# Performance work log

Measured on AMD Instinct MI355X. Metric: run time of the kernel, lower is better.

Reference implementation:

```python
import jax, jax.numpy as jnp
import numpy as np

B, S, D, E, K = 4, 2048, 1024, 8, 2
DF = 4 * D


def setup_inputs() -> dict:
    key = jax.random.key(0)
    ks = jax.random.split(key, 7)
    x = jax.random.normal(ks[0], (B, S, D), dtype=jnp.float32)
    Wr = jax.random.normal(ks[1], (D, E), dtype=jnp.float32) * 0.02
    br = jnp.zeros((E,), dtype=jnp.float32)
    W1 = jax.random.normal(ks[2], (E, D, DF), dtype=jnp.float32) * 0.02
    b1 = jnp.zeros((E, DF), dtype=jnp.float32)
    W2 = jax.random.normal(ks[3], (E, DF, D), dtype=jnp.float32) * 0.02
    b2 = jnp.zeros((E, D), dtype=jnp.float32)
    return {"x": x, "Wr": Wr, "br": br, "W1": W1, "b1": b1, "W2": W2, "b2": b2}


def reference(x, Wr, br, W1, b1, W2, b2):
    # Router: softmax gates then top-k
    gates = jax.nn.softmax(x @ Wr + br, axis=-1)               # [B,S,E]
    topk_vals, topk_idx = jax.lax.top_k(gates, K)              # [B,S,K]

    # Per-(token, expert) combine weight: gate value if expert selected else 0
    onehot = jax.nn.one_hot(topk_idx, E, dtype=gates.dtype)    # [B,S,K,E]
    combine = jnp.sum(onehot * topk_vals[..., None], axis=2)   # [B,S,E]

    # Expert MLPs (loop over fixed small expert count, fully vectorized per expert)
    output = jnp.zeros_like(x)
    for e in range(E):
        h = jax.nn.gelu(x @ W1[e] + b1[e], approximate=False)  # [B,S,4D]
        y = h @ W2[e] + b2[e]                                  # [B,S,D]
        output = output + combine[..., e:e + 1] * y

    # Load-balancing aux loss (dispatch mask: 1.0 where expert selected)
    dispatch = jnp.max(onehot, axis=2)                         # [B,S,E]
    mean_gates = gates.mean(axis=(0, 1))
    mean_dispatch = dispatch.mean(axis=(0, 1))
    aux_loss = jnp.sum(mean_gates * mean_dispatch) * E / (B * S)
    return output, aux_loss
```

## Files before the change

### kernel.cpp

```cpp
#include <hip/hip_runtime.h>
#include <hip/hip_bf16.h>
#include <hip/hip_fp16.h>

typedef _Float16 f16;
typedef _Float16 half8 __attribute__((ext_vector_type(8)));
typedef _Float16 half4 __attribute__((ext_vector_type(4)));
typedef float   floatx4 __attribute__((ext_vector_type(4)));

#define N_TOK   8192
#define D_DIM   1024
#define E_NUM   8
#define DF_DIM  4096
#define MAX_SLOTS 17408
#define MAX_RT    136

#define MI_COUNT  0
#define MI_CURSOR 8
#define MI_OFF    16
#define MI_TOTAL  25
#define MI_RTE    26
#define MI_SUMG   168

__device__ __forceinline__ void gld_lds16(const void* g, void* l) {
    __builtin_amdgcn_global_load_lds(
        (__attribute__((address_space(1))) const void*)g,
        (__attribute__((address_space(3))) void*)l, 16, 0, 0);
}

__device__ __forceinline__ float gelu_f(float v) {
    float u = 0.7978845608028654f * v * (1.0f + 0.044715f * v * v);
    float t = __expf(-2.0f * fabsf(u));
    float th = (1.0f - t) / (1.0f + t);
    th = (u >= 0.f) ? th : -th;
    return 0.5f * v * (1.0f + th);
}

__device__ __forceinline__ void transpose_tile(
    const float* __restrict__ src, f16* __restrict__ dst, int R, int C,
    int rb, int cb, float* tile )
{
    const int tid = threadIdx.x;
#pragma unroll
    for (int j = 0; j < 4; ++j) {
        int lin = j * 1024 + tid * 4;
        int r = lin >> 6, c = lin & 63;
        float4 v = *(const float4*)(src + (size_t)(rb + r) * C + (cb + c));
        tile[r * 65 + c + 0] = v.x; tile[r * 65 + c + 1] = v.y;
        tile[r * 65 + c + 2] = v.z; tile[r * 65 + c + 3] = v.w;
    }
    __syncthreads();
#pragma unroll
    for (int j = 0; j < 4; ++j) {
        int lin = j * 1024 + tid * 4;
        int c = lin >> 6, r = lin & 63;
        half4 o = { (f16)tile[(r + 0) * 65 + c], (f16)tile[(r + 1) * 65 + c],
                    (f16)tile[(r + 2) * 65 + c], (f16)tile[(r + 3) * 65 + c] };
        *(half4*)(dst + (size_t)(cb + c) * R + (rb + r)) = o;
    }
}

__global__ __launch_bounds__(256) void prep_kernel(
    const float* __restrict__ W1, f16* __restrict__ W1t,
    const float* __restrict__ x, const float* __restrict__ Wr,
    const float* __restrict__ br,
    int* __restrict__ topk_idx, float* __restrict__ topk_w,
    int* __restrict__ meta, f16* __restrict__ xh)
{
    __shared__ float tile[64 * 65];
    __shared__ float blk_sg[E_NUM];
    __shared__ int   blk_cnt[E_NUM];

    const int bid = blockIdx.x;
    if (bid < 8192) {
        const int cx = bid & 63, ry = (bid >> 6) & 15, ez = bid >> 10;
        transpose_tile(W1 + (size_t)ez * D_DIM * DF_DIM,
                       W1t + (size_t)ez * D_DIM * DF_DIM,
                       D_DIM, DF_DIM, ry * 64, cx * 64, tile);
        return;
    }

    const int rb = bid - 8192;
    const int w = threadIdx.x >> 6, l = threadIdx.x & 63;
    if (threadIdx.x < E_NUM) { blk_sg[threadIdx.x] = 0.f; blk_cnt[threadIdx.x] = 0; }
    __syncthreads();

    for (int it = 0; it < 4; ++it) {
        const int t = rb * 16 + w * 4 + it;
        const float* xr = x + (size_t)t * D_DIM + l * 16;
        float acc[E_NUM] = {0.f,0.f,0.f,0.f,0.f,0.f,0.f,0.f};
        f16 hx[16];
#pragma unroll
        for (int i = 0; i < 16; i += 4) {
            float4 xv = *(const float4*)(xr + i);
            const float xs[4] = {xv.x, xv.y, xv.z, xv.w};
#pragma unroll
            for (int jj = 0; jj < 4; ++jj) {
                hx[i + jj] = (f16)xs[jj];
                int d = l * 16 + i + jj;
                float4 w0 = *(const float4*)(Wr + (size_t)d * 8);
                float4 w1 = *(const float4*)(Wr + (size_t)d * 8 + 4);
                acc[0] += xs[jj] * w0.x; acc[1] += xs[jj] * w0.y;
                acc[2] += xs[jj] * w0.z; acc[3] += xs[jj] * w0.w;
                acc[4] += xs[jj] * w1.x; acc[5] += xs[jj] * w1.y;
                acc[6] += xs[jj] * w1.z; acc[7] += xs[jj] * w1.w;
            }
        }
        f16* xo = xh + (size_t)t * D_DIM + l * 16;
        *(half8*)(xo)     = *(const half8*)&hx[0];
        *(half8*)(xo + 8) = *(const half8*)&hx[8];
#pragma unroll
        for (int e = 0; e < E_NUM; ++e) {
#pragma unroll
            for (int off = 32; off > 0; off >>= 1)
                acc[e] += __shfl_down(acc[e], off);
        }
        if (l == 0) {
            float lg[E_NUM], g[E_NUM];
            float mx = -1e30f;
#pragma unroll
            for (int e = 0; e < E_NUM; ++e) { lg[e] = acc[e] + br[e]; mx = fmaxf(mx, lg[e]); }
            float sum = 0.f;
#pragma unroll
            for (int e = 0; e < E_NUM; ++e) { g[e] = __expf(lg[e] - mx); sum += g[e]; }
            float inv = 1.f / sum;
#pragma unroll
            for (int e = 0; e < E_NUM; ++e) g[e] *= inv;
            int e1 = 0; float v1 = g[0];
#pragma unroll
            for (int e = 1; e < E_NUM; ++e) if (g[e] > v1) { v1 = g[e]; e1 = e; }
            int e2 = -1; float v2 = -1.f;
#pragma unroll
            for (int e = 0; e < E_NUM; ++e) if (e != e1 && g[e] > v2) { v2 = g[e]; e2 = e; }
            topk_idx[t * 2 + 0] = e1; topk_idx[t * 2 + 1] = e2;
            topk_w[t * 2 + 0] = v1;   topk_w[t * 2 + 1] = v2;
#pragma unroll
            for (int e = 0; e < E_NUM; ++e) atomicAdd(&blk_sg[e], g[e]);
            atomicAdd(&blk_cnt[e1], 1); atomicAdd(&blk_cnt[e2], 1);
        }
    }
    __syncthreads();
    if (threadIdx.x < E_NUM) {
        atomicAdd((float*)(meta + MI_SUMG) + threadIdx.x, blk_sg[threadIdx.x]);
        atomicAdd(meta + MI_COUNT + threadIdx.x, blk_cnt[threadIdx.x]);
    }
}

__global__ __launch_bounds__(256) void fill_kernel(
    const int* __restrict__ topk_idx, const float* __restrict__ topk_w,
    int* __restrict__ meta, int* __restrict__ slot_token, float* __restrict__ slot_weight,
    int* __restrict__ slot_of, float* __restrict__ out_aux)
{
    __shared__ int offs[E_NUM + 1];
    const int tid = threadIdx.x;
    if (tid <= E_NUM) {
        int off = 0;
        for (int e = 0; e < tid; ++e)
            off += ((meta[MI_COUNT + e] + 127) >> 7) << 7;
        offs[tid] = off;
    }
    __syncthreads();

    const int t = blockIdx.x * 256 + tid;
#pragma unroll
    for (int k = 0; k < 2; ++k) {
        int e = topk_idx[t * 2 + k];
        int p = atomicAdd(meta + MI_CURSOR + e, 1);
        int slot = offs[e] + p;
        slot_token[slot] = t;
        slot_weight[slot] = topk_w[t * 2 + k];
        slot_of[t * 2 + k] = slot;
    }

    if (blockIdx.x == 0) {
        const int total = offs[E_NUM] >> 7;
        for (int rt = tid; rt < total; rt += 256) {
            int row = rt << 7, e = 0;
#pragma unroll
            for (int k = 1; k < E_NUM; ++k) if (row >= offs[k]) e = k;
            meta[MI_RTE + rt] = e;
        }
        for (int e = 0; e < E_NUM; ++e) {
            const int cnt = meta[MI_COUNT + e];
            const int hi = offs[e + 1];
            for (int i = offs[e] + cnt + tid; i < hi; i += 256) {
                slot_token[i] = 0;
                slot_weight[i] = 0.f;
            }
        }
        if (tid == 0) {
            meta[MI_TOTAL] = total;
            const float* sg = (const float*)(meta + MI_SUMG);
            float aux = 0.f;
            for (int e = 0; e < E_NUM; ++e)
                aux += (sg[e] / (float)N_TOK) * ((float)meta[MI_COUNT + e] / (float)N_TOK);
            out_aux[0] = aux * (float)E_NUM / (float)N_TOK;
        }
    }
}


template<int KD, int NCOLS, int KSPLIT, bool GATHER, bool GELU, bool BIAS, bool SWZ, bool FUSET>
__global__ __launch_bounds__(256, 4) void gemm128_kernel(
    const f16* __restrict__ A, const f16* __restrict__ Bw,
    const float* __restrict__ bias, const int* __restrict__ slot_token,
    const int* __restrict__ meta, f16* __restrict__ Out, size_t out_kp_stride,
    const float* __restrict__ Tsrc, f16* __restrict__ Tdst)
{
    constexpr int KLOC = KD / KSPLIT;
    constexpr int NT = KLOC / 64;
    __shared__ __align__(16) char smem_raw[32768];
    f16* As = (f16*)smem_raw;
    f16* Bs = (f16*)(smem_raw + 16384);

    if (FUSET && blockIdx.y >= MAX_RT) {
        const int id = (blockIdx.y - MAX_RT) * gridDim.x + blockIdx.x;
        const int cx = id & 15, ry = (id >> 4) & 63, ez = id >> 10;
        transpose_tile(Tsrc + (size_t)ez * D_DIM * DF_DIM,
                       Tdst + (size_t)ez * D_DIM * DF_DIM,
                       DF_DIM, D_DIM, ry * 64, cx * 64, (float*)smem_raw);
        return;
    }

    int nt, rt, kp;
    if (SWZ) {
        const int gx = gridDim.x, gy = gridDim.y;
        const int nwg = gx * gy * gridDim.z;
        const int flat = (blockIdx.z * gy + blockIdx.y) * gx + blockIdx.x;
        const int swz = (flat & 7) * (nwg >> 3) + (flat >> 3);
        nt = swz % gx;
        const int tmp = swz / gx;
        rt = tmp % gy;
        kp = tmp / gy;
    } else {
        nt = blockIdx.x; rt = blockIdx.y; kp = blockIdx.z;
    }

    if (rt >= meta[MI_TOTAL]) return;
    const int e  = meta[MI_RTE + rt];
    const int kbase = kp * KLOC;

    const int tid = threadIdx.x;
    const int w = tid >> 6, l = tid & 63;
    const int wr2 = w >> 1, wc2 = w & 1;
    const int fr = l & 15, fq = l >> 4;

    const int srow = tid >> 3;
    const int kcs  = (tid & 7) ^ (srow & 7);

    const f16* asrc[4]; const f16* bsrc[4];
#pragma unroll
    for (int i = 0; i < 4; ++i) {
        int r = i * 32 + srow;
        int ar;
        if (GATHER) ar = slot_token[rt * 128 + r];
        else        ar = rt * 128 + r;
        asrc[i] = A + (size_t)ar * KD + kbase + kcs * 8;
        bsrc[i] = Bw + ((size_t)e * NCOLS + (size_t)nt * 128 + r) * KD + kbase + kcs * 8;
    }

    const int rA  = wr2 * 64 + fr;
    const int rB  = wc2 * 64 + fr;
    const int sw0 = ( fq      ^ (fr & 7)) * 8;
    const int sw1 = ((4 + fq) ^ (fr & 7)) * 8;

    floatx4 acc[4][4];
#pragma unroll
    for (int m = 0; m < 4; ++m)
#pragma unroll
        for (int n = 0; n < 4; ++n) acc[m][n] = (floatx4){0.f, 0.f, 0.f, 0.f};

    half8 af[4], bf[4];

#pragma unroll 2
    for (int t = 0; t < NT; ++t) {
#pragma unroll
        for (int i = 0; i < 4; ++i) {
            gld_lds16(asrc[i] + (size_t)t * 64, &As[i * 2048 + tid * 8]);
            gld_lds16(bsrc[i] + (size_t)t * 64, &Bs[i * 2048 + tid * 8]);
        }
        asm volatile("s_waitcnt vmcnt(0)" ::: "memory");
        __builtin_amdgcn_s_barrier();
#pragma unroll
        for (int kk2 = 0; kk2 < 2; ++kk2) {
            const int sw = kk2 ? sw1 : sw0;
#pragma unroll
            for (int mj = 0; mj < 4; ++mj)
                af[mj] = *(const half8*)&As[(size_t)(rA + mj * 16) * 64 + sw];
#pragma unroll
            for (int nj = 0; nj < 4; ++nj)
                bf[nj] = *(const half8*)&Bs[(size_t)(rB + nj * 16) * 64 + sw];
#pragma unroll
            for (int mj = 0; mj < 4; ++mj)
#pragma unroll
                for (int nj = 0; nj < 4; ++nj)
                    acc[mj][nj] = __builtin_amdgcn_mfma_f32_16x16x32_f16(
                        af[mj], bf[nj], acc[mj][nj], 0, 0, 0);
        }
        __builtin_amdgcn_s_barrier();
    }

    f16* Op = Out + (size_t)kp * out_kp_stride;
    const int orow0 = rt * 128 + wr2 * 64;
    const int ocol0 = nt * 128 + wc2 * 64;
#pragma unroll
    for (int mj = 0; mj < 4; ++mj) {
#pragma unroll
        for (int nj = 0; nj < 4; ++nj) {
            const int col = ocol0 + nj * 16 + fr;
            float bs = 0.f;
            if (BIAS) bs = bias[(size_t)e * NCOLS + col];
#pragma unroll
            for (int j = 0; j < 4; ++j) {
                const int row = orow0 + mj * 16 + fq * 4 + j;
                float v = acc[mj][nj][j] + bs;
                if (GELU) v = gelu_f(v);
                Op[(size_t)row * NCOLS + col] = (f16)v;
            }
        }
    }
}

__global__ __launch_bounds__(256) void combine_kernel(
    const f16* __restrict__ P, const int* __restrict__ slot_of,
    const int* __restrict__ topk_idx, const float* __restrict__ topk_w,
    const float* __restrict__ b2, float* __restrict__ out)
{
    const int t = blockIdx.x;
    const int c = threadIdx.x;
    const size_t PS = (size_t)MAX_SLOTS * D_DIM;
    const int s0 = slot_of[t * 2], s1 = slot_of[t * 2 + 1];
    const int e0 = topk_idx[t * 2], e1 = topk_idx[t * 2 + 1];
    const float w0 = topk_w[t * 2], w1 = topk_w[t * 2 + 1];
    half4 a0 = *(const half4*)(P + (size_t)s0 * D_DIM + c * 4);
    half4 a1 = *(const half4*)(P + PS + (size_t)s0 * D_DIM + c * 4);
    half4 c0 = *(const half4*)(P + (size_t)s1 * D_DIM + c * 4);
    half4 c1 = *(const half4*)(P + PS + (size_t)s1 * D_DIM + c * 4);
    float4 bb0 = *(const float4*)(b2 + (size_t)e0 * D_DIM + c * 4);
    float4 bb1 = *(const float4*)(b2 + (size_t)e1 * D_DIM + c * 4);
    float4 o;
    o.x = w0 * ((float)a0[0] + (float)a1[0] + bb0.x) + w1 * ((float)c0[0] + (float)c1[0] + bb1.x);
    o.y = w0 * ((float)a0[1] + (float)a1[1] + bb0.y) + w1 * ((float)c0[1] + (float)c1[1] + bb1.y);
    o.z = w0 * ((float)a0[2] + (float)a1[2] + bb0.z) + w1 * ((float)c0[2] + (float)c1[2] + bb1.z);
    o.w = w0 * ((float)a0[3] + (float)a1[3] + bb0.w) + w1 * ((float)c0[3] + (float)c1[3] + bb1.w);
    *(float4*)(out + (size_t)t * D_DIM + c * 4) = o;
}

extern "C" void kernel_launch(void* const* d_in, const int* in_sizes, int n_in,
                              void* d_out, int out_size, void* d_ws, size_t ws_size,
                              hipStream_t stream) {
    const float* x  = (const float*)d_in[0];
    const float* Wr = (const float*)d_in[1];
    const float* br = (const float*)d_in[2];
    const float* W1 = (const float*)d_in[3];
    const float* b1 = (const float*)d_in[4];
    const float* W2 = (const float*)d_in[5];
    const float* b2 = (const float*)d_in[6];
    float* out = (float*)d_out;

    char* ws = (char*)d_ws;
    const size_t SZ_XH  = (size_t)N_TOK * D_DIM * 2;
    const size_t SZ_W1T = (size_t)E_NUM * DF_DIM * D_DIM * 2;
    const size_t SZ_W2T = SZ_W1T;
    const size_t SZ_H   = (size_t)MAX_SLOTS * DF_DIM * 2;

    f16* xh  = (f16*)(ws);
    f16* W1t = (f16*)(ws + SZ_XH);
    f16* W2t = (f16*)(ws + SZ_XH + SZ_W1T);
    f16* H   = (f16*)(ws + SZ_XH + SZ_W1T + SZ_W2T);
    f16* P   = (f16*)ws;
    char* p  = ws + SZ_XH + SZ_W1T + SZ_W2T + SZ_H;
    int*   topk_idx    = (int*)p;    p += (size_t)N_TOK * 2 * 4;
    float* topk_w      = (float*)p;  p += (size_t)N_TOK * 2 * 4;
    int*   slot_token  = (int*)p;    p += (size_t)MAX_SLOTS * 4;
    float* slot_weight = (float*)p;  p += (size_t)MAX_SLOTS * 4;
    int*   slot_of     = (int*)p;    p += (size_t)N_TOK * 2 * 4;
    int*   meta        = (int*)p;

    hipMemsetAsync(meta, 0, 1024, stream);

    prep_kernel<<<8704, 256, 0, stream>>>(
        W1, W1t, x, Wr, br, topk_idx, topk_w, meta, xh);

    fill_kernel<<<N_TOK / 256, 256, 0, stream>>>(
        topk_idx, topk_w, meta, slot_token, slot_weight, slot_of,
        out + (size_t)N_TOK * D_DIM);

    gemm128_kernel<D_DIM, DF_DIM, 1, true, true, true, false, true>
        <<<dim3(DF_DIM / 128, MAX_RT + 256, 1), 256, 0, stream>>>(
        xh, W1t, b1, slot_token, meta, H, 0, W2, W2t);

    gemm128_kernel<DF_DIM, D_DIM, 2, false, false, false, true, false>
        <<<dim3(D_DIM / 128, MAX_RT, 2), 256, 0, stream>>>(
        H, W2t, nullptr, slot_token, meta, P, (size_t)MAX_SLOTS * D_DIM, nullptr, nullptr);

    combine_kernel<<<N_TOK, 256, 0, stream>>>(P, slot_of, topk_idx, topk_w, b2, out);

    (void)in_sizes; (void)n_in; (void)ws_size;
}
```

Measured before the change: 514.8 us.

## Switch expert GEMMs to 256x256 tiles with double-buffered LDS pipeline

Replaces the 128x128 single-buffered GEMM with a 256x256-tile, 512-thread kernel that double-buffers A/B tiles in LDS and interleaves staged global-to-LDS loads with quarter-tile MFMA groups, using setprio around MFMA bursts. Expert slot padding changes from 128 to 256 rows to match, and the fused W2 transpose path is adapted to 512 threads. The aim is higher arithmetic intensity per LDS load and overlap of memory latency with compute. In exchange it uses 128KB LDS and large accumulator register pressure, lowers occupancy, and adds more padding rows per expert.

```diff
diff --git a/kernel.cpp b/kernel.cpp
--- a/kernel.cpp
+++ b/kernel.cpp
@@ -11,8 +11,8 @@
 #define D_DIM   1024
 #define E_NUM   8
 #define DF_DIM  4096
-#define MAX_SLOTS 17408
-#define MAX_RT    136
+#define MAX_SLOTS 18432
+#define MAX_RT    72
 
 #define MI_COUNT  0
 #define MI_CURSOR 8
@@ -33,30 +33,6 @@
     float th = (1.0f - t) / (1.0f + t);
     th = (u >= 0.f) ? th : -th;
     return 0.5f * v * (1.0f + th);
-}
-
-__device__ __forceinline__ void transpose_tile(
-    const float* __restrict__ src, f16* __restrict__ dst, int R, int C,
-    int rb, int cb, float* tile )
-{
-    const int tid = threadIdx.x;
-#pragma unroll
-    for (int j = 0; j < 4; ++j) {
-        int lin = j * 1024 + tid * 4;
-        int r = lin >> 6, c = lin & 63;
-        float4 v = *(const float4*)(src + (size_t)(rb + r) * C + (cb + c));
-        tile[r * 65 + c + 0] = v.x; tile[r * 65 + c + 1] = v.y;
-        tile[r * 65 + c + 2] = v.z; tile[r * 65 + c + 3] = v.w;
-    }
-    __syncthreads();
-#pragma unroll
-    for (int j = 0; j < 4; ++j) {
-        int lin = j * 1024 + tid * 4;
-        int c = lin >> 6, r = lin & 63;
-        half4 o = { (f16)tile[(r + 0) * 65 + c], (f16)tile[(r + 1) * 65 + c],
-                    (f16)tile[(r + 2) * 65 + c], (f16)tile[(r + 3) * 65 + c] };
-        *(half4*)(dst + (size_t)(cb + c) * R + (rb + r)) = o;
-    }
 }
 
 __global__ __launch_bounds__(256) void prep_kernel(
@@ -69,19 +45,37 @@
     __shared__ float tile[64 * 65];
     __shared__ float blk_sg[E_NUM];
     __shared__ int   blk_cnt[E_NUM];
+    const int tid = threadIdx.x;
 
     const int bid = blockIdx.x;
     if (bid < 8192) {
         const int cx = bid & 63, ry = (bid >> 6) & 15, ez = bid >> 10;
-        transpose_tile(W1 + (size_t)ez * D_DIM * DF_DIM,
-                       W1t + (size_t)ez * D_DIM * DF_DIM,
-                       D_DIM, DF_DIM, ry * 64, cx * 64, tile);
+        const float* s = W1 + (size_t)ez * D_DIM * DF_DIM;
+        f16* d = W1t + (size_t)ez * D_DIM * DF_DIM;
+        const int rb = ry * 64, cb = cx * 64;
+#pragma unroll
+        for (int j = 0; j < 4; ++j) {
+            int lin = j * 1024 + tid * 4;
+            int r = lin >> 6, c = lin & 63;
+            float4 v = *(const float4*)(s + (size_t)(rb + r) * DF_DIM + (cb + c));
+            tile[r * 65 + c + 0] = v.x; tile[r * 65 + c + 1] = v.y;
+            tile[r * 65 + c + 2] = v.z; tile[r * 65 + c + 3] = v.w;
+        }
+        __syncthreads();
+#pragma unroll
+        for (int j = 0; j < 4; ++j) {
+            int lin = j * 1024 + tid * 4;
+            int c = lin >> 6, r = lin & 63;
+            half4 o = { (f16)tile[(r + 0) * 65 + c], (f16)tile[(r + 1) * 65 + c],
+                        (f16)tile[(r + 2) * 65 + c], (f16)tile[(r + 3) * 65 + c] };
+            *(half4*)(d + (size_t)(cb + c) * D_DIM + (rb + r)) = o;
+        }
         return;
     }
 
     const int rb = bid - 8192;
-    const int w = threadIdx.x >> 6, l = threadIdx.x & 63;
-    if (threadIdx.x < E_NUM) { blk_sg[threadIdx.x] = 0.f; blk_cnt[threadIdx.x] = 0; }
+    const int w = tid >> 6, l = tid & 63;
+    if (tid < E_NUM) { blk_sg[tid] = 0.f; blk_cnt[tid] = 0; }
     __syncthreads();
 
     for (int it = 0; it < 4; ++it) {
@@ -139,9 +133,9 @@
         }
     }
     __syncthreads();
-    if (threadIdx.x < E_NUM) {
-        atomicAdd((float*)(meta + MI_SUMG) + threadIdx.x, blk_sg[threadIdx.x]);
-        atomicAdd(meta + MI_COUNT + threadIdx.x, blk_cnt[threadIdx.x]);
+    if (tid < E_NUM) {
+        atomicAdd((float*)(meta + MI_SUMG) + tid, blk_sg[tid]);
+        atomicAdd(meta + MI_COUNT + tid, blk_cnt[tid]);
     }
 }
 
@@ -155,7 +149,7 @@
     if (tid <= E_NUM) {
         int off = 0;
         for (int e = 0; e < tid; ++e)
-            off += ((meta[MI_COUNT + e] + 127) >> 7) << 7;
+            off += ((meta[MI_COUNT + e] + 255) >> 8) << 8;
         offs[tid] = off;
     }
     __syncthreads();
@@ -172,9 +166,9 @@
     }
 
     if (blockIdx.x == 0) {
-        const int total = offs[E_NUM] >> 7;
+        const int total = offs[E_NUM] >> 8;
         for (int rt = tid; rt < total; rt += 256) {
-            int row = rt << 7, e = 0;
+            int row = rt << 8, e = 0;
 #pragma unroll
             for (int k = 1; k < E_NUM; ++k) if (row >= offs[k]) e = k;
             meta[MI_RTE + rt] = e;
@@ -199,8 +193,47 @@
 }
 
 
+#define STG_A(T,H) do { int par_ = (T) & 1;                                     \
+    gld_lds16(aptr[H][0] + (size_t)(T) * 64,                                    \
+              &smem[par_ * 32768 + (H) * 8192 + tid * 8]);                      \
+    gld_lds16(aptr[H][1] + (size_t)(T) * 64,                                    \
+              &smem[par_ * 32768 + (H) * 8192 + 4096 + tid * 8]); } while(0)
+
+#define STG_B(T,H) do { int par_ = (T) & 1;                                     \
+    gld_lds16(bptr[H][0] + (size_t)(T) * 64,                                    \
+              &smem[par_ * 32768 + 16384 + (H) * 8192 + tid * 8]);              \
+    gld_lds16(bptr[H][1] + (size_t)(T) * 64,                                    \
+              &smem[par_ * 32768 + 16384 + (H) * 8192 + 4096 + tid * 8]); } while(0)
+
+#define RD_A(MH) do { _Pragma("unroll")                                         \
+    for (int mj = 0; mj < 4; ++mj) {                                            \
+        int lr = (MH) * 128 + wr2 * 64 + mj * 16 + fr;                          \
+        const f16* p_ = LA + (size_t)lr * 64;                                   \
+        af[mj][0] = *(const half8*)(p_ + ((fq)     ^ (lr & 7)) * 8);            \
+        af[mj][1] = *(const half8*)(p_ + ((4 + fq) ^ (lr & 7)) * 8);            \
+    } } while(0)
+
+#define RD_B(NH) do { _Pragma("unroll")                                         \
+    for (int nj = 0; nj < 2; ++nj) {                                            \
+        int lr = (NH) * 128 + wc2 * 32 + nj * 16 + fr;                          \
+        const f16* p_ = LB + (size_t)lr * 64;                                   \
+        bf[NH][nj][0] = *(const half8*)(p_ + ((fq)     ^ (lr & 7)) * 8);        \
+        bf[NH][nj][1] = *(const half8*)(p_ + ((4 + fq) ^ (lr & 7)) * 8);        \
+    } } while(0)
+
+#define MFMA8(MH,NH) do { __builtin_amdgcn_s_setprio(1);                        \
+    _Pragma("unroll")                                                           \
+    for (int mj = 0; mj < 4; ++mj) { _Pragma("unroll")                          \
+      for (int nj = 0; nj < 2; ++nj) {                                          \
+        acc[(MH)*4+mj][(NH)*2+nj] = __builtin_amdgcn_mfma_f32_16x16x32_f16(     \
+            af[mj][0], bf[NH][nj][0], acc[(MH)*4+mj][(NH)*2+nj], 0, 0, 0);      \
+        acc[(MH)*4+mj][(NH)*2+nj] = __builtin_amdgcn_mfma_f32_16x16x32_f16(     \
+            af[mj][1], bf[NH][nj][1], acc[(MH)*4+mj][(NH)*2+nj], 0, 0, 0);      \
+    } }                                                                         \
+    __builtin_amdgcn_s_setprio(0); } while(0)
+
 template<int KD, int NCOLS, int KSPLIT, bool GATHER, bool GELU, bool BIAS, bool SWZ, bool FUSET>
-__global__ __launch_bounds__(256, 4) void gemm128_kernel(
+__global__ __launch_bounds__(512, 2) void gemm256_kernel(
     const f16* __restrict__ A, const f16* __restrict__ Bw,
     const float* __restrict__ bias, const int* __restrict__ slot_token,
     const int* __restrict__ meta, f16* __restrict__ Out, size_t out_kp_stride,
@@ -208,16 +241,33 @@
 {
     constexpr int KLOC = KD / KSPLIT;
     constexpr int NT = KLOC / 64;
-    __shared__ __align__(16) char smem_raw[32768];
-    f16* As = (f16*)smem_raw;
-    f16* Bs = (f16*)(smem_raw + 16384);
+    __shared__ __align__(16) f16 smem[65536];
+    const int tid = threadIdx.x;
 
     if (FUSET && blockIdx.y >= MAX_RT) {
         const int id = (blockIdx.y - MAX_RT) * gridDim.x + blockIdx.x;
         const int cx = id & 15, ry = (id >> 4) & 63, ez = id >> 10;
-        transpose_tile(Tsrc + (size_t)ez * D_DIM * DF_DIM,
-                       Tdst + (size_t)ez * D_DIM * DF_DIM,
-                       DF_DIM, D_DIM, ry * 64, cx * 64, (float*)smem_raw);
+        float* tile = (float*)smem;
+        const float* s = Tsrc + (size_t)ez * D_DIM * DF_DIM;
+        f16* d = Tdst + (size_t)ez * D_DIM * DF_DIM;
+        const int rb = ry * 64, cb = cx * 64;
+#pragma unroll
+        for (int j = 0; j < 2; ++j) {
+            int lin = j * 2048 + tid * 4;
+            int r = lin >> 6, c = lin & 63;
+            float4 v = *(const float4*)(s + (size_t)(rb + r) * D_DIM + (cb + c));
+            tile[r * 65 + c + 0] = v.x; tile[r * 65 + c + 1] = v.y;
+            tile[r * 65 + c + 2] = v.z; tile[r * 65 + c + 3] = v.w;
+        }
+        __syncthreads();
+#pragma unroll
+        for (int j = 0; j < 2; ++j) {
+            int lin = j * 2048 + tid * 4;
+            int c = lin >> 6, r = lin & 63;
+            half4 o = { (f16)tile[(r + 0) * 65 + c], (f16)tile[(r + 1) * 65 + c],
+                        (f16)tile[(r + 2) * 65 + c], (f16)tile[(r + 3) * 65 + c] };
+            *(half4*)(d + (size_t)(cb + c) * DF_DIM + (rb + r)) = o;
+        }
         return;
     }
 
@@ -239,80 +289,83 @@
     const int e  = meta[MI_RTE + rt];
     const int kbase = kp * KLOC;
 
-    const int tid = threadIdx.x;
     const int w = tid >> 6, l = tid & 63;
-    const int wr2 = w >> 1, wc2 = w & 1;
+    const int wr2 = w >> 2, wc2 = w & 3;
     const int fr = l & 15, fq = l >> 4;
-
-    const int srow = tid >> 3;
-    const int kcs  = (tid & 7) ^ (srow & 7);
-
-    const f16* asrc[4]; const f16* bsrc[4];
-#pragma unroll
-    for (int i = 0; i < 4; ++i) {
-        int r = i * 32 + srow;
-        int ar;
-        if (GATHER) ar = slot_token[rt * 128 + r];
-        else        ar = rt * 128 + r;
-        asrc[i] = A + (size_t)ar * KD + kbase + kcs * 8;
-        bsrc[i] = Bw + ((size_t)e * NCOLS + (size_t)nt * 128 + r) * KD + kbase + kcs * 8;
-    }
-
-    const int rA  = wr2 * 64 + fr;
-    const int rB  = wc2 * 64 + fr;
-    const int sw0 = ( fq      ^ (fr & 7)) * 8;
-    const int sw1 = ((4 + fq) ^ (fr & 7)) * 8;
-
-    floatx4 acc[4][4];
-#pragma unroll
-    for (int m = 0; m < 4; ++m)
+    const int kcs = (tid & 7) ^ ((tid >> 3) & 7);
+
+    const f16* aptr[2][2]; const f16* bptr[2][2];
+#pragma unroll
+    for (int h = 0; h < 2; ++h) {
+#pragma unroll
+        for (int j = 0; j < 2; ++j) {
+            int arow = j * 128 + h * 64 + (tid >> 3);
+            int ga = GATHER ? slot_token[rt * 256 + arow] : rt * 256 + arow;
+            aptr[h][j] = A + (size_t)ga * KD + kbase + kcs * 8;
+            int loc = j * 64 + (tid >> 3);
+            int brow = (loc >> 5) * 64 + h * 32 + (loc & 31);
+            bptr[h][j] = Bw + ((size_t)e * NCOLS + (size_t)nt * 256 + brow) * KD + kbase + kcs * 8;
+        }
+    }
+
+    floatx4 acc[8][4];
+#pragma unroll
+    for (int m = 0; m < 8; ++m)
 #pragma unroll
         for (int n = 0; n < 4; ++n) acc[m][n] = (floatx4){0.f, 0.f, 0.f, 0.f};
 
-    half8 af[4], bf[4];
+    half8 af[4][2];
+    half8 bf[2][2][2];
+
+    STG_A(0, 0); STG_B(0, 0); STG_A(0, 1); STG_B(0, 1);
+    asm volatile("s_waitcnt vmcnt(4)" ::: "memory");
+    STG_A(1, 0); STG_B(1, 0); STG_A(1, 1);
+    asm volatile("s_waitcnt vmcnt(6)" ::: "memory");
+    __builtin_amdgcn_s_barrier();
 
 #pragma unroll 2
     for (int t = 0; t < NT; ++t) {
-#pragma unroll
-        for (int i = 0; i < 4; ++i) {
-            gld_lds16(asrc[i] + (size_t)t * 64, &As[i * 2048 + tid * 8]);
-            gld_lds16(bsrc[i] + (size_t)t * 64, &Bs[i * 2048 + tid * 8]);
-        }
-        asm volatile("s_waitcnt vmcnt(0)" ::: "memory");
-        __builtin_amdgcn_s_barrier();
-#pragma unroll
-        for (int kk2 = 0; kk2 < 2; ++kk2) {
-            const int sw = kk2 ? sw1 : sw0;
-#pragma unroll
-            for (int mj = 0; mj < 4; ++mj)
-                af[mj] = *(const half8*)&As[(size_t)(rA + mj * 16) * 64 + sw];
-#pragma unroll
-            for (int nj = 0; nj < 4; ++nj)
-                bf[nj] = *(const half8*)&Bs[(size_t)(rB + nj * 16) * 64 + sw];
-#pragma unroll
-            for (int mj = 0; mj < 4; ++mj)
-#pragma unroll
-                for (int nj = 0; nj < 4; ++nj)
-                    acc[mj][nj] = __builtin_amdgcn_mfma_f32_16x16x32_f16(
-                        af[mj], bf[nj], acc[mj][nj], 0, 0, 0);
-        }
-        __builtin_amdgcn_s_barrier();
+        const f16* LA = smem + (t & 1) * 32768;
+        const f16* LB = LA + 16384;
+        RD_A(0); RD_B(0);
+        if (t + 1 < NT) STG_B(t + 1, 1);
+        __builtin_amdgcn_s_barrier();
+        MFMA8(0, 0);
+        __builtin_amdgcn_s_barrier();
+        RD_B(1);
+        if (t + 2 < NT) STG_A(t + 2, 0);
+        __builtin_amdgcn_s_barrier();
+        MFMA8(0, 1);
+        __builtin_amdgcn_s_barrier();
+        RD_A(1);
+        if (t + 2 < NT) STG_B(t + 2, 0);
+        __builtin_amdgcn_s_barrier();
+        MFMA8(1, 0);
+        __builtin_amdgcn_s_barrier();
+        if (t + 2 < NT) STG_A(t + 2, 1);
+        __builtin_amdgcn_s_barrier();
+        MFMA8(1, 1);
+        if (t + 1 < NT) {
+            if (t + 2 < NT) asm volatile("s_waitcnt vmcnt(6)" ::: "memory");
+            else            asm volatile("s_waitcnt vmcnt(0)" ::: "memory");
+            __builtin_amdgcn_s_barrier();
+        }
     }
 
     f16* Op = Out + (size_t)kp * out_kp_stride;
-    const int orow0 = rt * 128 + wr2 * 64;
-    const int ocol0 = nt * 128 + wc2 * 64;
-#pragma unroll
-    for (int mj = 0; mj < 4; ++mj) {
-#pragma unroll
-        for (int nj = 0; nj < 4; ++nj) {
-            const int col = ocol0 + nj * 16 + fr;
+    const int orow0 = rt * 256 + wr2 * 128;
+    const int ocol0 = nt * 256 + wc2 * 64;
+#pragma unroll
+    for (int mi = 0; mi < 8; ++mi) {
+#pragma unroll
+        for (int ni = 0; ni < 4; ++ni) {
+            const int col = ocol0 + (ni >> 1) * 32 + (ni & 1) * 16 + fr;
             float bs = 0.f;
             if (BIAS) bs = bias[(size_t)e * NCOLS + col];
 #pragma unroll
             for (int j = 0; j < 4; ++j) {
-                const int row = orow0 + mj * 16 + fq * 4 + j;
-                float v = acc[mj][nj][j] + bs;
+                const int row = orow0 + (mi >> 2) * 64 + (mi & 3) * 16 + fq * 4 + j;
+                float v = acc[mi][ni][j] + bs;
                 if (GELU) v = gelu_f(v);
                 Op[(size_t)row * NCOLS + col] = (f16)v;
             }
@@ -385,12 +438,12 @@
         topk_idx, topk_w, meta, slot_token, slot_weight, slot_of,
         out + (size_t)N_TOK * D_DIM);
 
-    gemm128_kernel<D_DIM, DF_DIM, 1, true, true, true, false, true>
-        <<<dim3(DF_DIM / 128, MAX_RT + 256, 1), 256, 0, stream>>>(
+    gemm256_kernel<D_DIM, DF_DIM, 1, true, true, true, false, true>
+        <<<dim3(DF_DIM / 256, MAX_RT + 512, 1), 512, 0, stream>>>(
         xh, W1t, b1, slot_token, meta, H, 0, W2, W2t);
 
-    gemm128_kernel<DF_DIM, D_DIM, 2, false, false, false, true, false>
-        <<<dim3(D_DIM / 128, MAX_RT, 2), 256, 0, stream>>>(
+    gemm256_kernel<DF_DIM, D_DIM, 2, false, false, false, true, false>
+        <<<dim3(D_DIM / 256, MAX_RT, 2), 512, 0, stream>>>(
         H, W2t, nullptr, slot_token, meta, P, (size_t)MAX_SLOTS * D_DIM, nullptr, nullptr);
 
     combine_kernel<<<N_TOK, 256, 0, stream>>>(P, slot_of, topk_idx, topk_w, b2, out);
```

Result: slower. 560.4 us (+8.9%).
